# Kernel tuning notes

Hardware: AMD Instinct MI355X
Metric: run time of the kernel (lower is better)

## Reference

```python
import jax, jax.numpy as jnp
import numpy as np

D = 1024      # hidden_dim
E = 8         # num_experts
H = 4096      # expert_hidden_dim (= 4*D, module default)
K = 2         # top-k experts per token


def setup_inputs() -> dict:
    key = jax.random.key(0)
    ks = jax.random.split(key, 7)
    s = 1.0 / np.sqrt(D)
    sh = 1.0 / np.sqrt(H)
    return {
        "x": jax.random.normal(ks[0], (4, 1024, D), dtype=jnp.float32),
        "W1": jax.random.uniform(ks[1], (E, D, H), jnp.float32, -s, s),
        "b1": jax.random.uniform(ks[2], (E, H), jnp.float32, -s, s),
        "W2": jax.random.uniform(ks[3], (E, H, D), jnp.float32, -sh, sh),
        "b2": jax.random.uniform(ks[4], (E, D), jnp.float32, -sh, sh),
        "Wg": jax.random.uniform(ks[5], (D, E), jnp.float32, -s, s),
        "bg": jax.random.uniform(ks[6], (E,), jnp.float32, -s, s),
    }


def reference(x, W1, b1, W2, b2, Wg, bg):
    orig_shape = x.shape
    x2d = x.reshape(-1, D)                                    # [N, D]
    gate_scores = jax.nn.softmax(x2d @ Wg + bg, axis=-1)      # [N, E]
    topk_scores, topk_idx = jax.lax.top_k(gate_scores, K)     # [N, K]
    # Dense all-experts 2-layer MLP (dropout is identity in eval mode)
    h = jax.nn.gelu(jnp.einsum('nd,edh->neh', x2d, W1) + b1[None], approximate=False)  # [N, E, H]
    expert_out = jnp.einsum('neh,ehd->ned', h, W2) + b2[None]  # [N, E, D]
    # Gather top-k expert outputs and combine with gate weights
    topk_out = jnp.take_along_axis(expert_out, topk_idx[:, :, None], axis=1)  # [N, K, D]
    out = jnp.sum(topk_out * topk_scores[:, :, None], axis=1)  # [N, D]
    return out.reshape(orig_shape)
```

## Files before the change

kernel.cpp:

```cpp
#include <hip/hip_runtime.h>
#include <math.h>

#define DIM  1024
#define NEXP 8
#define HID  4096
#define TOPK 2

typedef __attribute__((ext_vector_type(8))) short bf16x8;
typedef __attribute__((ext_vector_type(4))) float f32x4;

__device__ inline unsigned short f2bf(float f) {
  union { float f; unsigned int u; } v; v.f = f;
  unsigned int u = v.u;
  return (unsigned short)((u + 0x7FFFu + ((u >> 16) & 1u)) >> 16);
}

__device__ inline void load_lds16(const void* g, void* l) {
  __builtin_amdgcn_global_load_lds(
      (const __attribute__((address_space(1))) void*)g,
      (__attribute__((address_space(3))) void*)l, 16, 0, 0);
}

__device__ inline float gelu_f(float v) {
  float x = v * 0.70710678118654752f;
  float ax = fabsf(x);
  float t = 1.f / (1.f + 0.3275911f * ax);
  float poly = t * (0.254829592f + t * (-0.284496736f + t * (1.421413741f +
               t * (-1.453152027f + t * 1.061405429f))));
  float er = 1.f - poly * __expf(-ax * ax);
  er = (x < 0.f) ? -er : er;
  return 0.5f * v * (1.f + er);
}

__global__ void gate_kernel(const float* __restrict__ x,
                            const float* __restrict__ Wg,
                            const float* __restrict__ bg,
                            float* __restrict__ topk_score,
                            int* __restrict__ count,
                            int* __restrict__ lists,
                            int N) {
  int n = blockIdx.x;
  if (n >= N) return;
  int lane = threadIdx.x;
  float acc[NEXP];
#pragma unroll
  for (int e = 0; e < NEXP; ++e) acc[e] = 0.f;
  const float* xr = x + (size_t)n * DIM;
  for (int d = lane; d < DIM; d += 64) {
    float xv = xr[d];
    const float* w = Wg + (size_t)d * NEXP;
#pragma unroll
    for (int e = 0; e < NEXP; ++e) acc[e] += xv * w[e];
  }
#pragma unroll
  for (int off = 32; off > 0; off >>= 1) {
#pragma unroll
    for (int e = 0; e < NEXP; ++e) acc[e] += __shfl_xor(acc[e], off, 64);
  }
  if (lane == 0) {
    float l[NEXP];
#pragma unroll
    for (int e = 0; e < NEXP; ++e) l[e] = acc[e] + bg[e];
    float m = l[0];
#pragma unroll
    for (int e = 1; e < NEXP; ++e) m = fmaxf(m, l[e]);
    float p[NEXP];
    float s = 0.f;
#pragma unroll
    for (int e = 0; e < NEXP; ++e) { p[e] = expf(l[e] - m); s += p[e]; }
    int i0 = 0;
#pragma unroll
    for (int e = 1; e < NEXP; ++e) if (l[e] > l[i0]) i0 = e;
    int i1 = (i0 == 0) ? 1 : 0;
#pragma unroll
    for (int e = 0; e < NEXP; ++e) if (e != i0 && l[e] > l[i1]) i1 = e;
    float inv = 1.f / s;
    topk_score[n * TOPK + 0] = p[i0] * inv;
    topk_score[n * TOPK + 1] = p[i1] * inv;
    int pos0 = atomicAdd(&count[i0], 1);
    lists[(size_t)i0 * N + pos0] = n * TOPK + 0;
    int pos1 = atomicAdd(&count[i1], 1);
    lists[(size_t)i1 * N + pos1] = n * TOPK + 1;
  }
}

__global__ void offsets_kernel(const int* __restrict__ count, int* __restrict__ offsets,
                               int* __restrict__ tiles, int* __restrict__ ntiles) {
  if (threadIdx.x == 0 && blockIdx.x == 0) {
    int s = 0, nt = 0;
    for (int e = 0; e < NEXP; ++e) {
      offsets[e] = s;
      int c = count[e];
      s += c;
      int rts = (c + 127) >> 7;
      for (int i = 0; i < rts; ++i) tiles[nt++] = (e << 16) | i;
    }
    offsets[NEXP] = s;
    ntiles[0] = nt;
  }
}

template <int TILED>
__global__ void gather_kernel(const float* __restrict__ x,
                              const int* __restrict__ offsets,
                              const int* __restrict__ lists,
                              unsigned short* __restrict__ Xg,
                              int* __restrict__ pairmap,
                              int N, int NPAD) {
  int g = blockIdx.x;
  int e = 0;
  while (e < NEXP - 1 && g >= offsets[e + 1]) ++e;
  int i = g - offsets[e];
  int ent = lists[(size_t)e * N + i];
  int tok = ent >> 1;
  if (threadIdx.x == 0) pairmap[g] = ent;
  int d0 = threadIdx.x * 4;
  float4 v = *((const float4*)(x + (size_t)tok * DIM + d0));
  ushort4 o;
  o.x = f2bf(v.x); o.y = f2bf(v.y); o.z = f2bf(v.z); o.w = f2bf(v.w);
  if (TILED) {
    *(ushort4*)(Xg + ((size_t)(d0 >> 6) * NPAD + g) * 64 + (d0 & 63)) = o;
  } else {
    *(ushort4*)(Xg + (size_t)g * DIM + d0) = o;
  }
}

__global__ __launch_bounds__(256) void transpose_convert_t(
    const float* __restrict__ src, unsigned short* __restrict__ dst, int R, int C) {
  const int e = blockIdx.z;
  src += (size_t)e * R * C;
  dst += (size_t)e * R * C;
  const int r0 = blockIdx.x * 64, c0 = blockIdx.y * 64;
  __shared__ unsigned short Ts[64][68];
  const int t = threadIdx.x;
  const int rr = t >> 4, cc = (t & 15) * 4;
#pragma unroll
  for (int p = 0; p < 4; ++p) {
    int r = rr + p * 16;
    float4 v = *(const float4*)(src + (size_t)(r0 + r) * C + c0 + cc);
    Ts[cc + 0][r] = f2bf(v.x);
    Ts[cc + 1][r] = f2bf(v.y);
    Ts[cc + 2][r] = f2bf(v.z);
    Ts[cc + 3][r] = f2bf(v.w);
  }
  __syncthreads();
  const int cr = t >> 3, rq = (t & 7) * 8;
  const size_t kbbase = (size_t)(r0 >> 6) * C;
#pragma unroll
  for (int p = 0; p < 2; ++p) {
    int c = cr + p * 32;
    ushort4 a = *(ushort4*)&Ts[c][rq];
    ushort4 b = *(ushort4*)&Ts[c][rq + 4];
    unsigned short* dp = dst + (kbbase + (c0 + c)) * 64 + rq;
    *(ushort4*)(dp) = a;
    *(ushort4*)(dp + 4) = b;
  }
}

template <int PASS>
__global__ __launch_bounds__(256) void moe_gemm14(
    const unsigned short* __restrict__ Asrc,
    const unsigned short* __restrict__ Bt,
    const float* __restrict__ bias,
    const int* __restrict__ offsets,
    const int* __restrict__ tiles,
    const int* __restrict__ ntiles,
    const int* __restrict__ pairmap,
    const float* __restrict__ score,
    unsigned short* __restrict__ Hmat,
    float* __restrict__ out,
    int maxt, int NPAD) {
  constexpr int K  = (PASS == 1) ? DIM : HID;
  constexpr int NS = (PASS == 1) ? HID : DIM;
  constexpr int KS = (PASS == 1) ? 1 : 2;
  constexpr int KL = K / KS;
  constexpr int NT = KL / 32;
  constexpr int KBK = K / 64;

  const unsigned orig = blockIdx.x;
  const unsigned nwg = gridDim.x;
  const unsigned q = nwg >> 3, r8 = nwg & 7;
  const unsigned xcd = orig & 7, p8 = orig >> 3;
  const unsigned id = (xcd < r8 ? xcd * (q + 1) : r8 * (q + 1) + (xcd - r8) * q) + p8;
  const int tt = (int)(id % (unsigned)maxt);
  const int ct = (int)(id / (unsigned)maxt);

  if (tt >= ntiles[0]) return;
  const int pk = tiles[tt];
  const int e  = pk >> 16;
  const int rt = pk & 0xffff;
  const int gbase = offsets[e];
  const int nc = offsets[e + 1] - gbase;
  const int rowsvalid = min(128, nc - rt * 128);
  const int kz = (PASS == 1) ? 0 : blockIdx.z;
  const int kb0 = (kz * KL) >> 6;

  __shared__ unsigned short As[128 * 32];
  __shared__ unsigned short Bs[128 * 32];

  const int tid  = threadIdx.x;
  const int lane = tid & 63;
  const int wid  = tid >> 6;
  const int wr = (wid >> 1) * 64;
  const int wc = (wid & 1) * 64;
  const int fr = lane & 15;
  const int fq = lane >> 4;

  f32x4 acc[4][4];
#pragma unroll
  for (int m = 0; m < 4; ++m)
#pragma unroll
    for (int n = 0; n < 4; ++n) acc[m][n] = (f32x4){0.f, 0.f, 0.f, 0.f};

  const unsigned short* Ab = Asrc + ((size_t)kb0 * NPAD + (gbase + rt * 128)) * 64;
  const unsigned short* Bb = Bt + (((size_t)e * KBK + kb0) * NS + (size_t)ct * 128) * 64;

  for (int t = 0; t < NT; ++t) {
    {
      const unsigned short* ga = Ab + (size_t)(t >> 1) * ((size_t)NPAD * 64) + (t & 1) * 32;
      const unsigned short* gb = Bb + (size_t)(t >> 1) * ((size_t)NS * 64) + (t & 1) * 32;
#pragma unroll
      for (int i = 0; i < 2; ++i) {
        const int c = i * 256 + tid;
        const int row = c >> 2;
        const int u = c & 3;
        load_lds16(ga + (size_t)row * 64 + u * 8, (char*)As + c * 16);
        load_lds16(gb + (size_t)row * 64 + u * 8, (char*)Bs + c * 16);
      }
    }
    __syncthreads();

    {
      bf16x8 af[4], bf[4];
#pragma unroll
      for (int m = 0; m < 4; ++m)
        af[m] = *(const bf16x8*)&As[(wr + m * 16 + fr) * 32 + fq * 8];
#pragma unroll
      for (int n = 0; n < 4; ++n)
        bf[n] = *(const bf16x8*)&Bs[(wc + n * 16 + fr) * 32 + fq * 8];
#pragma unroll
      for (int m = 0; m < 4; ++m)
#pragma unroll
        for (int n = 0; n < 4; ++n)
          acc[m][n] = __builtin_amdgcn_mfma_f32_16x16x32_bf16(af[m], bf[n], acc[m][n], 0, 0, 0);
    }
    __syncthreads();
  }

  if (PASS == 1) {
    const size_t cb = (size_t)(ct * 2 + (wc >> 6));
#pragma unroll
    for (int n = 0; n < 4; ++n) {
      const int col = ct * 128 + wc + n * 16 + fr;
      const int cl = n * 16 + fr;
      const float b1v = bias[(size_t)e * NS + col];
#pragma unroll
      for (int m = 0; m < 4; ++m) {
#pragma unroll
        for (int r = 0; r < 4; ++r) {
          const int lrow = wr + m * 16 + fq * 4 + r;
          if (lrow < rowsvalid) {
            float v = gelu_f(acc[m][n][r] + b1v);
            Hmat[(cb * NPAD + (gbase + rt * 128 + lrow)) * 64 + cl] = f2bf(v);
          }
        }
      }
    }
  } else {
    float b2v[4];
#pragma unroll
    for (int n = 0; n < 4; ++n)
      b2v[n] = (kz == 0) ? bias[(size_t)e * NS + ct * 128 + wc + n * 16 + fr] : 0.f;
#pragma unroll
    for (int m = 0; m < 4; ++m) {
#pragma unroll
      for (int r = 0; r < 4; ++r) {
        const int lrow = wr + m * 16 + fq * 4 + r;
        if (lrow < rowsvalid) {
          const int g = gbase + rt * 128 + lrow;
          const int ent = pairmap[g];
          const int tok = ent >> 1;
          const float s = score[ent];
#pragma unroll
          for (int n = 0; n < 4; ++n) {
            const int col = ct * 128 + wc + n * 16 + fr;
            atomicAdd(&out[(size_t)tok * DIM + col], s * (acc[m][n][r] + b2v[n]));
          }
        }
      }
    }
  }
}

template <int PASS>
__global__ __launch_bounds__(256) void moe_gemm(
    const unsigned short* __restrict__ Asrc,
    const float* __restrict__ Bsrc,
    const float* __restrict__ bias,
    const int* __restrict__ offsets,
    const int* __restrict__ pairmap,
    const float* __restrict__ score,
    unsigned short* __restrict__ Hmat,
    float* __restrict__ out) {
  constexpr int K  = (PASS == 1) ? DIM : HID;
  constexpr int NS = (PASS == 1) ? HID : DIM;
  const int e = blockIdx.z;
  const int gbase = offsets[e];
  const int nc = offsets[e + 1] - gbase;
  const int rt = blockIdx.x;
  if (rt * 128 >= nc) return;
  const int rowsvalid = min(128, nc - rt * 128);
  const int ct = blockIdx.y;
  __shared__ unsigned short As[128 * 40];
  __shared__ unsigned short Bs[128 * 40];
  const int tid  = threadIdx.x;
  const int lane = tid & 63;
  const int wid  = tid >> 6;
  const int wr = (wid >> 1) * 64;
  const int wc = (wid & 1) * 64;
  const int fr = lane & 15;
  const int fq = lane >> 4;
  f32x4 acc[4][4];
#pragma unroll
  for (int m = 0; m < 4; ++m)
#pragma unroll
    for (int n = 0; n < 4; ++n) acc[m][n] = (f32x4){0.f, 0.f, 0.f, 0.f};
  const int ar = tid >> 1;
  const int ak = (tid & 1) * 16;
  int arow = rt * 128 + ((ar < rowsvalid) ? ar : 0);
  const unsigned short* Aptr = Asrc + (size_t)(gbase + arow) * K + ak;
  const int bc = (tid & 31) * 4;
  const int bk = (tid >> 5) * 4;
  const float* Bptr = Bsrc + (size_t)e * K * NS + (size_t)bk * NS + ct * 128 + bc;
  for (int k0 = 0; k0 < K; k0 += 32) {
    uint4 av0 = *(const uint4*)(Aptr + k0);
    uint4 av1 = *(const uint4*)(Aptr + k0 + 8);
    const float* bp = Bptr + (size_t)k0 * NS;
    float4 w0 = *(const float4*)(bp);
    float4 w1 = *(const float4*)(bp + NS);
    float4 w2 = *(const float4*)(bp + 2 * NS);
    float4 w3 = *(const float4*)(bp + 3 * NS);
    __syncthreads();
    *(uint4*)&As[ar * 40 + ak]     = av0;
    *(uint4*)&As[ar * 40 + ak + 8] = av1;
    {
      uint2 pv;
      pv.x = (unsigned int)f2bf(w0.x) | ((unsigned int)f2bf(w1.x) << 16);
      pv.y = (unsigned int)f2bf(w2.x) | ((unsigned int)f2bf(w3.x) << 16);
      *(uint2*)&Bs[(bc + 0) * 40 + bk] = pv;
      pv.x = (unsigned int)f2bf(w0.y) | ((unsigned int)f2bf(w1.y) << 16);
      pv.y = (unsigned int)f2bf(w2.y) | ((unsigned int)f2bf(w3.y) << 16);
      *(uint2*)&Bs[(bc + 1) * 40 + bk] = pv;
      pv.x = (unsigned int)f2bf(w0.z) | ((unsigned int)f2bf(w1.z) << 16);
      pv.y = (unsigned int)f2bf(w2.z) | ((unsigned int)f2bf(w3.z) << 16);
      *(uint2*)&Bs[(bc + 2) * 40 + bk] = pv;
      pv.x = (unsigned int)f2bf(w0.w) | ((unsigned int)f2bf(w1.w) << 16);
      pv.y = (unsigned int)f2bf(w0.w) | ((unsigned int)f2bf(w3.w) << 16);
      pv.x = (unsigned int)f2bf(w0.w) | ((unsigned int)f2bf(w1.w) << 16);
      pv.y = (unsigned int)f2bf(w2.w) | ((unsigned int)f2bf(w3.w) << 16);
      *(uint2*)&Bs[(bc + 3) * 40 + bk] = pv;
    }
    __syncthreads();
    bf16x8 af[4], bfr[4];
#pragma unroll
    for (int m = 0; m < 4; ++m)
      af[m] = *(const bf16x8*)&As[(wr + m * 16 + fr) * 40 + fq * 8];
#pragma unroll
    for (int n = 0; n < 4; ++n)
      bfr[n] = *(const bf16x8*)&Bs[(wc + n * 16 + fr) * 40 + fq * 8];
#pragma unroll
    for (int m = 0; m < 4; ++m)
#pragma unroll
      for (int n = 0; n < 4; ++n)
        acc[m][n] = __builtin_amdgcn_mfma_f32_16x16x32_bf16(af[m], bfr[n], acc[m][n], 0, 0, 0);
  }
  if (PASS == 1) {
#pragma unroll
    for (int n = 0; n < 4; ++n) {
      int col = ct * 128 + wc + n * 16 + fr;
      float b1v = bias[(size_t)e * NS + col];
#pragma unroll
      for (int m = 0; m < 4; ++m) {
#pragma unroll
        for (int r = 0; r < 4; ++r) {
          int lrow = wr + m * 16 + fq * 4 + r;
          if (lrow < rowsvalid) {
            float v = acc[m][n][r] + b1v;
            v = 0.5f * v * (1.f + erff(v * 0.70710678118654752440f));
            Hmat[(size_t)(gbase + rt * 128 + lrow) * HID + col] = f2bf(v);
          }
        }
      }
    }
  } else {
    float b2v[4];
#pragma unroll
    for (int n = 0; n < 4; ++n)
      b2v[n] = bias[(size_t)e * NS + ct * 128 + wc + n * 16 + fr];
#pragma unroll
    for (int m = 0; m < 4; ++m) {
#pragma unroll
      for (int r = 0; r < 4; ++r) {
        int lrow = wr + m * 16 + fq * 4 + r;
        if (lrow < rowsvalid) {
          int g = gbase + rt * 128 + lrow;
          int ent = pairmap[g];
          int tok = ent >> 1;
          float s = score[ent];
#pragma unroll
          for (int n = 0; n < 4; ++n) {
            int col = ct * 128 + wc + n * 16 + fr;
            atomicAdd(&out[(size_t)tok * DIM + col], s * (acc[m][n][r] + b2v[n]));
          }
        }
      }
    }
  }
}

extern "C" void kernel_launch(void* const* d_in, const int* in_sizes, int n_in,
                              void* d_out, int out_size, void* d_ws, size_t ws_size,
                              hipStream_t stream) {
  const float* x  = (const float*)d_in[0];
  const float* W1 = (const float*)d_in[1];
  const float* b1 = (const float*)d_in[2];
  const float* W2 = (const float*)d_in[3];
  const float* b2 = (const float*)d_in[4];
  const float* Wg = (const float*)d_in[5];
  const float* bg = (const float*)d_in[6];
  float* out = (float*)d_out;
  const int N  = in_sizes[0] / DIM;
  const int NP = N * TOPK;
  const int NPAD = NP + 256;
  const int MAXT = NP / 128 + NEXP;

  char* ws = (char*)d_ws;
  size_t off = 0;
  auto alloc = [&](size_t bytes) -> void* {
    void* p = ws + off;
    off = (off + bytes + 255) & ~(size_t)255;
    return p;
  };
  int*   count      = (int*)alloc(NEXP * sizeof(int));
  int*   offsets    = (int*)alloc((NEXP + 1) * sizeof(int));
  int*   tiles      = (int*)alloc((size_t)MAXT * sizeof(int));
  int*   ntiles     = (int*)alloc(sizeof(int));
  float* topk_score = (float*)alloc((size_t)NP * sizeof(float));
  int*   lists      = (int*)alloc((size_t)NEXP * N * sizeof(int));
  int*   pairmap    = (int*)alloc((size_t)NP * sizeof(int));
  unsigned short* Xg   = (unsigned short*)alloc((size_t)NPAD * DIM * sizeof(unsigned short));
  unsigned short* Hmat = (unsigned short*)alloc((size_t)NPAD * HID * sizeof(unsigned short));
  unsigned short* W1T = (unsigned short*)alloc((size_t)NEXP * DIM * HID * sizeof(unsigned short));
  unsigned short* W2T = (unsigned short*)alloc((size_t)NEXP * HID * DIM * sizeof(unsigned short));
  size_t need_full = off;

  hipMemsetAsync(count, 0, NEXP * sizeof(int), stream);
  gate_kernel<<<N, 64, 0, stream>>>(x, Wg, bg, topk_score, count, lists, N);
  offsets_kernel<<<1, 64, 0, stream>>>(count, offsets, tiles, ntiles);
  hipMemsetAsync(out, 0, (size_t)out_size * sizeof(float), stream);

  if (ws_size >= need_full) {
    gather_kernel<1><<<NP, DIM / 4, 0, stream>>>(x, offsets, lists, Xg, pairmap, N, NPAD);
    dim3 tg1(DIM / 64, HID / 64, NEXP);
    transpose_convert_t<<<tg1, 256, 0, stream>>>(W1, W1T, DIM, HID);
    dim3 tg2(HID / 64, DIM / 64, NEXP);
    transpose_convert_t<<<tg2, 256, 0, stream>>>(W2, W2T, HID, DIM);

    dim3 g1((HID / 128) * MAXT, 1, 1);
    moe_gemm14<1><<<g1, 256, 0, stream>>>(Xg, W1T, b1, offsets, tiles, ntiles,
                                          pairmap, topk_score, Hmat, out, MAXT, NPAD);
    dim3 g2((DIM / 128) * MAXT, 1, 2);
    moe_gemm14<2><<<g2, 256, 0, stream>>>(Hmat, W2T, b2, offsets, tiles, ntiles,
                                          pairmap, topk_score, Hmat, out, MAXT, NPAD);
  } else {
    gather_kernel<0><<<NP, DIM / 4, 0, stream>>>(x, offsets, lists, Xg, pairmap, N, NPAD);
    const int RT = (N + 127) / 128;
    dim3 g1(RT, HID / 128, NEXP);
    moe_gemm<1><<<g1, 256, 0, stream>>>(Xg, W1, b1, offsets, pairmap, topk_score, Hmat, out);
    dim3 g2(RT, DIM / 128, NEXP);
    moe_gemm<2><<<g2, 256, 0, stream>>>(Hmat, W2, b2, offsets, pairmap, topk_score, Hmat, out);
  }
}
```

Before: 518.1 us.

## Double-buffer LDS tiles in grouped MoE GEMM and merge weight transposes

The grouped GEMM now keeps two LDS buffers, so the async global-to-LDS load for the next K step is issued while MFMAs run on the current one. This also drops one barrier per iteration. The two per-weight transpose/convert launches are merged into one kernel in which each block handles four 64-column subtiles, cutting launch count and block overhead. The cost is twice the LDS per block, which may lower occupancy. A redundant duplicate line in the fallback path is also removed.

```diff
diff --git a/kernel.cpp b/kernel.cpp
--- a/kernel.cpp
+++ b/kernel.cpp
@@ -125,40 +125,59 @@
   }
 }
 
-__global__ __launch_bounds__(256) void transpose_convert_t(
-    const float* __restrict__ src, unsigned short* __restrict__ dst, int R, int C) {
-  const int e = blockIdx.z;
-  src += (size_t)e * R * C;
-  dst += (size_t)e * R * C;
-  const int r0 = blockIdx.x * 64, c0 = blockIdx.y * 64;
+__global__ __launch_bounds__(256) void transpose_convert_all(
+    const float* __restrict__ W1, const float* __restrict__ W2,
+    unsigned short* __restrict__ W1T, unsigned short* __restrict__ W2T) {
+  int idx = blockIdx.x;
+  const float* src; unsigned short* dst; int C, r0, c0base;
+  if (idx < 2048) {
+    const int e = idx >> 8, rem = idx & 255;
+    C = 4096;
+    r0 = (rem >> 4) * 64;
+    c0base = (rem & 15) * 256;
+    src = W1 + (size_t)e * 1024 * 4096;
+    dst = W1T + (size_t)e * 1024 * 4096;
+  } else {
+    idx -= 2048;
+    const int e = idx >> 8, rem = idx & 255;
+    C = 1024;
+    r0 = (rem >> 2) * 64;
+    c0base = (rem & 3) * 256;
+    src = W2 + (size_t)e * 4096 * 1024;
+    dst = W2T + (size_t)e * 4096 * 1024;
+  }
   __shared__ unsigned short Ts[64][68];
   const int t = threadIdx.x;
   const int rr = t >> 4, cc = (t & 15) * 4;
-#pragma unroll
-  for (int p = 0; p < 4; ++p) {
-    int r = rr + p * 16;
-    float4 v = *(const float4*)(src + (size_t)(r0 + r) * C + c0 + cc);
-    Ts[cc + 0][r] = f2bf(v.x);
-    Ts[cc + 1][r] = f2bf(v.y);
-    Ts[cc + 2][r] = f2bf(v.z);
-    Ts[cc + 3][r] = f2bf(v.w);
-  }
-  __syncthreads();
   const int cr = t >> 3, rq = (t & 7) * 8;
   const size_t kbbase = (size_t)(r0 >> 6) * C;
-#pragma unroll
-  for (int p = 0; p < 2; ++p) {
-    int c = cr + p * 32;
-    ushort4 a = *(ushort4*)&Ts[c][rq];
-    ushort4 b = *(ushort4*)&Ts[c][rq + 4];
-    unsigned short* dp = dst + (kbbase + (c0 + c)) * 64 + rq;
-    *(ushort4*)(dp) = a;
-    *(ushort4*)(dp + 4) = b;
+  for (int sub = 0; sub < 4; ++sub) {
+    const int c0 = c0base + sub * 64;
+#pragma unroll
+    for (int p = 0; p < 4; ++p) {
+      int r = rr + p * 16;
+      float4 v = *(const float4*)(src + (size_t)(r0 + r) * C + c0 + cc);
+      Ts[cc + 0][r] = f2bf(v.x);
+      Ts[cc + 1][r] = f2bf(v.y);
+      Ts[cc + 2][r] = f2bf(v.z);
+      Ts[cc + 3][r] = f2bf(v.w);
+    }
+    __syncthreads();
+#pragma unroll
+    for (int p = 0; p < 2; ++p) {
+      int c = cr + p * 32;
+      ushort4 a = *(ushort4*)&Ts[c][rq];
+      ushort4 b = *(ushort4*)&Ts[c][rq + 4];
+      unsigned short* dp = dst + (kbbase + (c0 + c)) * 64 + rq;
+      *(ushort4*)(dp) = a;
+      *(ushort4*)(dp + 4) = b;
+    }
+    __syncthreads();
   }
 }
 
 template <int PASS>
-__global__ __launch_bounds__(256) void moe_gemm14(
+__global__ __launch_bounds__(256) void moe_gemm15(
     const unsigned short* __restrict__ Asrc,
     const unsigned short* __restrict__ Bt,
     const float* __restrict__ bias,
@@ -195,8 +214,8 @@
   const int kz = (PASS == 1) ? 0 : blockIdx.z;
   const int kb0 = (kz * KL) >> 6;
 
-  __shared__ unsigned short As[128 * 32];
-  __shared__ unsigned short Bs[128 * 32];
+  __shared__ unsigned short As[2][128 * 32];
+  __shared__ unsigned short Bs[2][128 * 32];
 
   const int tid  = threadIdx.x;
   const int lane = tid & 63;
@@ -215,36 +234,38 @@
   const unsigned short* Ab = Asrc + ((size_t)kb0 * NPAD + (gbase + rt * 128)) * 64;
   const unsigned short* Bb = Bt + (((size_t)e * KBK + kb0) * NS + (size_t)ct * 128) * 64;
 
+  auto stage = [&](int b, int t) {
+    const unsigned short* ga = Ab + (size_t)(t >> 1) * ((size_t)NPAD * 64) + (t & 1) * 32;
+    const unsigned short* gb = Bb + (size_t)(t >> 1) * ((size_t)NS * 64) + (t & 1) * 32;
+#pragma unroll
+    for (int i = 0; i < 2; ++i) {
+      const int c = i * 256 + tid;
+      const int row = c >> 2;
+      const int u = c & 3;
+      load_lds16(ga + (size_t)row * 64 + u * 8, (char*)As[b] + c * 16);
+      load_lds16(gb + (size_t)row * 64 + u * 8, (char*)Bs[b] + c * 16);
+    }
+  };
+
+  stage(0, 0);
+
   for (int t = 0; t < NT; ++t) {
-    {
-      const unsigned short* ga = Ab + (size_t)(t >> 1) * ((size_t)NPAD * 64) + (t & 1) * 32;
-      const unsigned short* gb = Bb + (size_t)(t >> 1) * ((size_t)NS * 64) + (t & 1) * 32;
-#pragma unroll
-      for (int i = 0; i < 2; ++i) {
-        const int c = i * 256 + tid;
-        const int row = c >> 2;
-        const int u = c & 3;
-        load_lds16(ga + (size_t)row * 64 + u * 8, (char*)As + c * 16);
-        load_lds16(gb + (size_t)row * 64 + u * 8, (char*)Bs + c * 16);
-      }
-    }
     __syncthreads();
-
-    {
-      bf16x8 af[4], bf[4];
-#pragma unroll
-      for (int m = 0; m < 4; ++m)
-        af[m] = *(const bf16x8*)&As[(wr + m * 16 + fr) * 32 + fq * 8];
+    if (t + 1 < NT) stage((t + 1) & 1, t + 1);
+    const unsigned short* Ac = As[t & 1];
+    const unsigned short* Bc = Bs[t & 1];
+    bf16x8 af[4], bf[4];
+#pragma unroll
+    for (int m = 0; m < 4; ++m)
+      af[m] = *(const bf16x8*)&Ac[(wr + m * 16 + fr) * 32 + fq * 8];
+#pragma unroll
+    for (int n = 0; n < 4; ++n)
+      bf[n] = *(const bf16x8*)&Bc[(wc + n * 16 + fr) * 32 + fq * 8];
+#pragma unroll
+    for (int m = 0; m < 4; ++m)
 #pragma unroll
       for (int n = 0; n < 4; ++n)
-        bf[n] = *(const bf16x8*)&Bs[(wc + n * 16 + fr) * 32 + fq * 8];
-#pragma unroll
-      for (int m = 0; m < 4; ++m)
-#pragma unroll
-        for (int n = 0; n < 4; ++n)
-          acc[m][n] = __builtin_amdgcn_mfma_f32_16x16x32_bf16(af[m], bf[n], acc[m][n], 0, 0, 0);
-    }
-    __syncthreads();
+        acc[m][n] = __builtin_amdgcn_mfma_f32_16x16x32_bf16(af[m], bf[n], acc[m][n], 0, 0, 0);
   }
 
   if (PASS == 1) {
@@ -355,8 +376,6 @@
       pv.y = (unsigned int)f2bf(w2.z) | ((unsigned int)f2bf(w3.z) << 16);
       *(uint2*)&Bs[(bc + 2) * 40 + bk] = pv;
       pv.x = (unsigned int)f2bf(w0.w) | ((unsigned int)f2bf(w1.w) << 16);
-      pv.y = (unsigned int)f2bf(w0.w) | ((unsigned int)f2bf(w3.w) << 16);
-      pv.x = (unsigned int)f2bf(w0.w) | ((unsigned int)f2bf(w1.w) << 16);
       pv.y = (unsigned int)f2bf(w2.w) | ((unsigned int)f2bf(w3.w) << 16);
       *(uint2*)&Bs[(bc + 3) * 40 + bk] = pv;
     }
@@ -461,16 +480,13 @@
 
   if (ws_size >= need_full) {
     gather_kernel<1><<<NP, DIM / 4, 0, stream>>>(x, offsets, lists, Xg, pairmap, N, NPAD);
-    dim3 tg1(DIM / 64, HID / 64, NEXP);
-    transpose_convert_t<<<tg1, 256, 0, stream>>>(W1, W1T, DIM, HID);
-    dim3 tg2(HID / 64, DIM / 64, NEXP);
-    transpose_convert_t<<<tg2, 256, 0, stream>>>(W2, W2T, HID, DIM);
+    transpose_convert_all<<<4096, 256, 0, stream>>>(W1, W2, W1T, W2T);
 
     dim3 g1((HID / 128) * MAXT, 1, 1);
-    moe_gemm14<1><<<g1, 256, 0, stream>>>(Xg, W1T, b1, offsets, tiles, ntiles,
+    moe_gemm15<1><<<g1, 256, 0, stream>>>(Xg, W1T, b1, offsets, tiles, ntiles,
                                           pairmap, topk_score, Hmat, out, MAXT, NPAD);
     dim3 g2((DIM / 128) * MAXT, 1, 2);
-    moe_gemm14<2><<<g2, 256, 0, stream>>>(Hmat, W2T, b2, offsets, tiles, ntiles,
+    moe_gemm15<2><<<g2, 256, 0, stream>>>(Hmat, W2T, b2, offsets, tiles, ntiles,
                                           pairmap, topk_score, Hmat, out, MAXT, NPAD);
   } else {
     gather_kernel<0><<<NP, DIM / 4, 0, stream>>>(x, offsets, lists, Xg, pairmap, N, NPAD);
```

Result: slower. 536.6 us (+3.6%).
